# Optimization experiments

Measured on AMD Instinct MI355X. Metric: run time of the kernel, lower is better.

Reference implementation:

```python
import jax, jax.numpy as jnp
import numpy as np

N_GRAPHS = 128   # number of graphs in the batch
G = 128          # nodes per graph (equal-sized ragged blocks for the reference)
D = 512          # node embedding dim (feature_dim)
EPS = 1e-7


def setup_inputs() -> dict:
    key = jax.random.key(0)
    embeddings = jax.random.normal(key, (N_GRAPHS * G, D), dtype=jnp.float32)
    # Precompute block-diagonal strict-upper-triangular mask as gather indices.
    # Equivalent to torch.block_diag(*[triu(ones(g,g), diagonal=1) for g in sizes]).bool()
    iu_r, iu_c = np.triu_indices(G, k=1)                 # per-block triu(.,1) indices
    offsets = (np.arange(N_GRAPHS) * G)[:, None]         # block offsets into [N, N]
    row_idx = jnp.asarray((offsets + iu_r[None, :]).ravel(), dtype=jnp.int32)
    col_idx = jnp.asarray((offsets + iu_c[None, :]).ravel(), dtype=jnp.int32)
    return {"embeddings": embeddings, "row_idx": row_idx, "col_idx": col_idx}


def reference(embeddings, row_idx, col_idx):
    # Full NxN dot-product similarity (N = total nodes across all graphs).
    sims = embeddings @ embeddings.T                     # [N, N]
    m = sims.min()
    M = sims.max()
    sims = (sims - m) / (M - m + EPS)                    # global min-max normalization
    # Gather block-diagonal strict-upper-triangular entries -> flat vector.
    return sims[row_idx, col_idx]                        # [sum_g g*(g-1)/2]
```

## Files before the change

### kernel.cpp

```cpp
#include <hip/hip_runtime.h>
#include <hip/hip_bf16.h>
#include <stdint.h>


typedef __attribute__((ext_vector_type(8))) __bf16 bf16x8;
typedef __attribute__((ext_vector_type(16))) float floatx16;
typedef __attribute__((ext_vector_type(4))) int intx4;
typedef __attribute__((ext_vector_type(16))) int intx16;

#define AS1 __attribute__((address_space(1)))
#define AS3 __attribute__((address_space(3)))

static constexpr int DIM      = 512;
static constexpr int SLOTX    = 40;
static constexpr int NSLOT    = SLOTX * 64;
static constexpr float QS     = 19.5f;
static constexpr int MARGIN_I = 3042;


static __device__ __forceinline__ unsigned short f2bf_rne(float f) {
  unsigned int u = __float_as_uint(f);
  u += 0x7fffu + ((u >> 16) & 1u);
  return (unsigned short)(u >> 16);
}
static __device__ __forceinline__ int fkey(float f) {
  int s = __float_as_int(f);
  return s >= 0 ? s : (s ^ 0x7fffffff);
}
static __device__ __forceinline__ float funkey(int k) {
  return __int_as_float(k >= 0 ? k : (k ^ 0x7fffffff));
}
static __device__ __forceinline__ int swzd(int row, int c16) {
  return c16 ^ (row & 15);
}
static __device__ __forceinline__ int swz8(int row, int c8) {
  return c8 ^ (row & 7);
}
static __device__ __forceinline__ int qswap(int v) {
  return (v & 0x7A) | ((v & 1) << 2) | ((v >> 2) & 1);
}
static __device__ __forceinline__ int sfun(int row) {
  return (row & 3) ^ ((row >> 3) & 3);
}

__global__ void k_convert(const float* __restrict__ in,
                          unsigned short* __restrict__ bf,
                          char* __restrict__ q,
                          int* __restrict__ ctrl, int n4) {
  int i = blockIdx.x * blockDim.x + threadIdx.x;
  if (i == 0) {
    ctrl[0] = 0x7fffffff; ctrl[1] = (int)0x80000000;
    ctrl[2] = 0x7fffffff;
  }
  if (i >= n4) return;
  float4 v = ((const float4*)in)[i];
  ushort4 o;
  o.x = f2bf_rne(v.x); o.y = f2bf_rne(v.y);
  o.z = f2bf_rne(v.z); o.w = f2bf_rne(v.w);
  ((ushort4*)bf)[i] = o;
  int qx = __float2int_rn(v.x * QS), qy = __float2int_rn(v.y * QS);
  int qz = __float2int_rn(v.z * QS), qw = __float2int_rn(v.w * QS);
  char4 c;
  c.x = (char)min(127, max(-127, qx));
  c.y = (char)min(127, max(-127, qy));
  c.z = (char)min(127, max(-127, qz));
  c.w = (char)min(127, max(-127, qw));
  ((char4*)q)[i] = c;
}

__global__ __launch_bounds__(512, 2) void k_gemm(
    const char* __restrict__ Eq,
    const unsigned short* __restrict__ E,
    int* __restrict__ ipart,
    float* __restrict__ diagblocks,
    int* __restrict__ ctrl) {
  const int x = blockIdx.x;
  const int y = blockIdx.y;
  if (x > 34) return;
  const int pi = y * SLOTX + x;

  const int tid = threadIdx.x;
  __shared__ __align__(16) char smem[2][32768];
  __shared__ float2 redbuf[8];
  __shared__ int iredbuf[8];

  const int w = tid >> 6, lane = tid & 63;
  const int l31 = lane & 31;
  const int kg  = lane >> 5;

  if (x < 33) {
    const int tt = (y + x) & 63;
    const int rA0 = 256 * y,  rA1 = 256 * y + 128;
    const int rB0 = 256 * tt, rB1 = 256 * tt + 128;

    const int wr = w >> 1, wc = w & 1;

    intx16 acc[2][4];
#pragma unroll
    for (int i = 0; i < 2; i++)
#pragma unroll
      for (int j = 0; j < 4; j++)
#pragma unroll
        for (int r = 0; r < 16; r++) acc[i][j][r] = 0;

#define STAGE4(bb, kt) do {                                                   \
    int q_   = tid >> 2;                                                      \
    int row_ = qswap(q_);                                                     \
    int off_ = (kt) * 64 + (((tid & 3) ^ sfun(row_)) * 16);                   \
    char* d_ = smem[bb] + tid * 16;                                           \
    __builtin_amdgcn_global_load_lds(                                         \
        (const AS1 unsigned int*)(Eq + (size_t)(rA0 + row_) * DIM + off_),    \
        (AS3 unsigned int*)d_, 16, 0, 0);                                     \
    __builtin_amdgcn_global_load_lds(                                         \
        (const AS1 unsigned int*)(Eq + (size_t)(rA1 + row_) * DIM + off_),    \
        (AS3 unsigned int*)(d_ + 8192), 16, 0, 0);                            \
    __builtin_amdgcn_global_load_lds(                                         \
        (const AS1 unsigned int*)(Eq + (size_t)(rB0 + row_) * DIM + off_),    \
        (AS3 unsigned int*)(d_ + 16384), 16, 0, 0);                           \
    __builtin_amdgcn_global_load_lds(                                         \
        (const AS1 unsigned int*)(Eq + (size_t)(rB1 + row_) * DIM + off_),    \
        (AS3 unsigned int*)(d_ + 24576), 16, 0, 0);                           \
  } while (0)

    const int ra0 = wr * 64 + l31, ra1 = wr * 64 + 32 + l31;
    const int pa0 = (ra0 >> 7) * 8192 + qswap(ra0 & 127) * 64, sa0 = sfun(ra0 & 127);
    const int pa1 = (ra1 >> 7) * 8192 + qswap(ra1 & 127) * 64, sa1 = sfun(ra1 & 127);
    const int rb0 = 0 * 32 + l31, rb1 = 1 * 32 + l31;
    const int rb2 = 2 * 32 + l31, rb3 = 3 * 32 + l31;
    const int pbB = 16384 + wc * 8192;
    const int pb0 = pbB + qswap(rb0) * 64, sb0 = sfun(rb0);
    const int pb1 = pbB + qswap(rb1) * 64, sb1 = sfun(rb1);
    const int pb2 = pbB + qswap(rb2) * 64, sb2 = sfun(rb2);
    const int pb3 = pbB + qswap(rb3) * 64, sb3 = sfun(rb3);

    STAGE4(0, 0);
    __syncthreads();

#pragma unroll
    for (int kt = 0; kt < 8; kt++) {
      if (kt + 1 < 8) STAGE4((kt + 1) & 1, kt + 1);
      const char* cb = smem[kt & 1];
#pragma unroll
      for (int ks = 0; ks < 2; ks++) {
        const int c = ks * 2 + kg;
        intx4 af0 = *(const intx4*)(cb + pa0 + ((c ^ sa0) << 4));
        intx4 af1 = *(const intx4*)(cb + pa1 + ((c ^ sa1) << 4));
        intx4 b0  = *(const intx4*)(cb + pb0 + ((c ^ sb0) << 4));
        intx4 b1  = *(const intx4*)(cb + pb1 + ((c ^ sb1) << 4));
        intx4 b2  = *(const intx4*)(cb + pb2 + ((c ^ sb2) << 4));
        intx4 b3  = *(const intx4*)(cb + pb3 + ((c ^ sb3) << 4));
        acc[0][0] = __builtin_amdgcn_mfma_i32_32x32x32_i8(af0, b0, acc[0][0], 0, 0, 0);
        acc[0][1] = __builtin_amdgcn_mfma_i32_32x32x32_i8(af0, b1, acc[0][1], 0, 0, 0);
        acc[0][2] = __builtin_amdgcn_mfma_i32_32x32x32_i8(af0, b2, acc[0][2], 0, 0, 0);
        acc[0][3] = __builtin_amdgcn_mfma_i32_32x32x32_i8(af0, b3, acc[0][3], 0, 0, 0);
        acc[1][0] = __builtin_amdgcn_mfma_i32_32x32x32_i8(af1, b0, acc[1][0], 0, 0, 0);
        acc[1][1] = __builtin_amdgcn_mfma_i32_32x32x32_i8(af1, b1, acc[1][1], 0, 0, 0);
        acc[1][2] = __builtin_amdgcn_mfma_i32_32x32x32_i8(af1, b2, acc[1][2], 0, 0, 0);
        acc[1][3] = __builtin_amdgcn_mfma_i32_32x32x32_i8(af1, b3, acc[1][3], 0, 0, 0);
      }
      __syncthreads();
    }
#undef STAGE4

    int vmin = 0x7fffffff;
#pragma unroll
    for (int ti = 0; ti < 2; ti++)
#pragma unroll
      for (int tj = 0; tj < 4; tj++)
#pragma unroll
        for (int r = 0; r < 16; r++) vmin = min(vmin, acc[ti][tj][r]);
#pragma unroll
    for (int m_ = 32; m_ >= 1; m_ >>= 1)
      vmin = min(vmin, __shfl_xor(vmin, m_));
    if (lane == 0) iredbuf[w] = vmin;
    __syncthreads();
    if (tid == 0) {
      int mn = iredbuf[0];
      for (int i = 1; i < 8; i++) mn = min(mn, iredbuf[i]);
      ipart[pi] = mn;
      atomicMin(&ctrl[2], mn);
    }
  } else {
    if (tid == 0) ipart[pi] = 0x7fffffff;
    const int tr = 2 * y + (x - 33);
    unsigned short* lA = (unsigned short*)&smem[0][0];
    const int wr = w >> 2, wcq = w & 3;
    floatx16 acc[2];
#pragma unroll
    for (int t = 0; t < 2; t++)
#pragma unroll
      for (int r = 0; r < 16; r++) acc[t][r] = 0.f;

    const int rowBase = tr * 128;

    for (int kb = 0; kb < 4; kb++) {
      const int kBase = kb * 128;
#pragma unroll
      for (int j = 0; j < 4; j++) {
        int p   = j * 512 + tid;
        int row = p >> 4, c16 = p & 15;
        int sc = swzd(row, c16);
        const unsigned short* gA =
            E + (size_t)(rowBase + row) * DIM + kBase + sc * 8;
        __builtin_amdgcn_global_load_lds((const AS1 unsigned int*)gA,
                                         (AS3 unsigned int*)(lA + p * 8), 16, 0, 0);
      }
      __syncthreads();

#pragma unroll
      for (int ks = 0; ks < 8; ks++) {
        bf16x8 af[2], bfv;
        const int c16 = ks * 2 + kg;
#pragma unroll
        for (int t = 0; t < 2; t++) {
          int ra = wr * 64 + t * 32 + l31;
          af[t]  = *(const bf16x8*)(lA + ra * 128 + swzd(ra, c16) * 8);
        }
        {
          int rb = wcq * 32 + l31;
          bfv = *(const bf16x8*)(lA + rb * 128 + swzd(rb, c16) * 8);
        }
#pragma unroll
        for (int t = 0; t < 2; t++)
          acc[t] = __builtin_amdgcn_mfma_f32_32x32x16_bf16(
              af[t], bfv, acc[t], 0, 0, 0);
      }
      __syncthreads();
    }

    float vmin = 3.4e38f, vmax = -3.4e38f;
#pragma unroll
    for (int t = 0; t < 2; t++)
#pragma unroll
      for (int r = 0; r < 16; r++) {
        float v = acc[t][r];
        vmin = fminf(vmin, v);
        vmax = fmaxf(vmax, v);
      }
#pragma unroll
    for (int m_ = 32; m_ >= 1; m_ >>= 1) {
      vmin = fminf(vmin, __shfl_xor(vmin, m_));
      vmax = fmaxf(vmax, __shfl_xor(vmax, m_));
    }
    if (lane == 0) redbuf[w] = make_float2(vmin, vmax);
    __syncthreads();
    if (tid == 0) {
      float mn = redbuf[0].x, mx = redbuf[0].y;
      for (int i = 1; i < 8; i++) {
        mn = fminf(mn, redbuf[i].x);
        mx = fmaxf(mx, redbuf[i].y);
      }
      atomicMin(&ctrl[0], fkey(mn));
      atomicMax(&ctrl[1], fkey(mx));
    }

    float* Bout = diagblocks + (size_t)tr * (128 * 128);
    const int cbase = wcq * 32 + l31;
#pragma unroll
    for (int t = 0; t < 2; t++) {
#pragma unroll
      for (int r = 0; r < 16; r++) {
        int row = wr * 64 + t * 32 + (r & 3) + 8 * (r >> 2) + 4 * kg;
        Bout[row * 128 + cbase] = acc[t][r];
      }
    }
  }
}

__global__ __launch_bounds__(256) void k_refine(
    const unsigned short* __restrict__ E,
    const int* __restrict__ ipart, int* __restrict__ ctrl) {
  const int pi = blockIdx.x;
  if (ipart[pi] > ctrl[2] + MARGIN_I) return;
  const int y = pi / SLOTX, x = pi % SLOTX;
  if (x >= 33) return;
  const int tt = (y + x) & 63;

  const int tid = threadIdx.x;
  __shared__ __align__(16) unsigned short lA[128 * 64];
  __shared__ __align__(16) unsigned short lB[128 * 64];
  __shared__ float redbuf[4];

  const int w = tid >> 6, lane = tid & 63;
  const int wr = w >> 1, wc = w & 1;
  const int l31 = lane & 31;
  const int kg  = lane >> 5;

  for (int ab = 0; ab < 4; ab++) {
    const int rowBaseA = (2 * y + (ab >> 1)) * 128;
    const int rowBaseB = (2 * tt + (ab & 1)) * 128;

    floatx16 acc[2][2];
#pragma unroll
    for (int i = 0; i < 2; i++)
#pragma unroll
      for (int j = 0; j < 2; j++)
#pragma unroll
        for (int r = 0; r < 16; r++) acc[i][j][r] = 0.f;

    for (int kb = 0; kb < 8; kb++) {
      const int kBase = kb * 64;
#pragma unroll
      for (int j = 0; j < 4; j++) {
        int cb  = (w * 4 + j) * 64;
        int p   = cb + lane;
        int row = p >> 3, c8 = p & 7;
        int sc8 = swz8(row, c8);
        const unsigned short* gA = E + (size_t)(rowBaseA + row) * DIM + kBase + sc8 * 8;
        const unsigned short* gB = E + (size_t)(rowBaseB + row) * DIM + kBase + sc8 * 8;
        __builtin_amdgcn_global_load_lds((const AS1 unsigned int*)gA,
                                         (AS3 unsigned int*)(lA + cb * 8), 16, 0, 0);
        __builtin_amdgcn_global_load_lds((const AS1 unsigned int*)gB,
                                         (AS3 unsigned int*)(lB + cb * 8), 16, 0, 0);
      }
      __syncthreads();

#pragma unroll
      for (int ks = 0; ks < 4; ks++) {
        bf16x8 af[2], bfv[2];
        const int c8 = ks * 2 + kg;
#pragma unroll
        for (int t = 0; t < 2; t++) {
          int ra = wr * 64 + t * 32 + l31;
          int rb = wc * 64 + t * 32 + l31;
          af[t]  = *(const bf16x8*)(lA + (ra * 8 + swz8(ra, c8)) * 8);
          bfv[t] = *(const bf16x8*)(lB + (rb * 8 + swz8(rb, c8)) * 8);
        }
#pragma unroll
        for (int ti = 0; ti < 2; ti++)
#pragma unroll
          for (int tj = 0; tj < 2; tj++)
            acc[ti][tj] = __builtin_amdgcn_mfma_f32_32x32x16_bf16(
                af[ti], bfv[tj], acc[ti][tj], 0, 0, 0);
      }
      __syncthreads();
    }

    float vmin = 3.4e38f;
#pragma unroll
    for (int ti = 0; ti < 2; ti++)
#pragma unroll
      for (int tj = 0; tj < 2; tj++)
#pragma unroll
        for (int r = 0; r < 16; r++) vmin = fminf(vmin, acc[ti][tj][r]);
#pragma unroll
    for (int m_ = 32; m_ >= 1; m_ >>= 1)
      vmin = fminf(vmin, __shfl_xor(vmin, m_));
    if (lane == 0) redbuf[w] = vmin;
    __syncthreads();
    if (tid == 0) {
      float mn = redbuf[0];
      for (int i = 1; i < 4; i++) mn = fminf(mn, redbuf[i]);
      atomicMin(&ctrl[0], fkey(mn));
    }
    __syncthreads();
  }
}

__global__ __launch_bounds__(256) void k_gather(
    const int* __restrict__ rix, const int* __restrict__ cix,
    const float* __restrict__ blocks, const int* __restrict__ ctrl,
    float* __restrict__ out, int n) {
  int i = blockIdx.x * blockDim.x + threadIdx.x;
  if (i >= n) return;
  float m   = funkey(ctrl[0]);
  float M   = funkey(ctrl[1]);
  float inv = 1.0f / (M - m + 1e-7f);
  int r = rix[i], c = cix[i];
  int g = r >> 7;
  float v = blocks[((size_t)g << 14) + ((r & 127) << 7) + (c & 127)];
  out[i] = (v - m) * inv;
}

extern "C" void kernel_launch(void* const* d_in, const int* in_sizes, int n_in,
                              void* d_out, int out_size, void* d_ws, size_t ws_size,
                              hipStream_t stream) {
  const float* emb = (const float*)d_in[0];
  const int* rix   = (const int*)d_in[1];
  const int* cix   = (const int*)d_in[2];

  char* ws = (char*)d_ws;
  int* ctrl           = (int*)ws;
  unsigned short* Ebf = (unsigned short*)(ws + 256);
  char* Eq            = (char*)(ws + 256 + (16u << 20));
  float* diagblocks   = (float*)(ws + 256 + (24u << 20));
  int* ipart          = (int*)(ws + 256 + (32u << 20));
  int n4 = in_sizes[0] / 4;

  k_convert<<<(n4 + 255) / 256, 256, 0, stream>>>(emb, Ebf, Eq, ctrl, n4);

  k_gemm<<<dim3(SLOTX, 64), 512, 0, stream>>>(Eq, Ebf, ipart, diagblocks, ctrl);

  k_refine<<<NSLOT, 256, 0, stream>>>(Ebf, ipart, ctrl);

  k_gather<<<(out_size + 255) / 256, 256, 0, stream>>>(rix, cix, diagblocks,
                                                       ctrl, (float*)d_out,
                                                       out_size);
}
```

Baseline: 200.1 us.

## Triple-buffer int8 GEMM tiles with split staging and explicit waitcnt barriers

Moves the int8 GEMM mainloop from double to triple LDS buffering. Tiles are now prefetched two k-steps ahead, and each stage's global-to-LDS loads are split across the two inner k-substeps. __syncthreads is replaced with manual s_barrier, vmcnt/lgkmcnt waits, sched_barrier and setprio around the MFMA bursts, to hide load latency and interleave loads with compute. The cost is 96KB of LDS per block, which may cut occupancy below the two blocks per CU requested by launch_bounds, plus fragile hand-tuned wait counts.

After: 206.0 us. +2.9%, slower.

```diff
diff --git a/kernel.cpp b/kernel.cpp
--- a/kernel.cpp
+++ b/kernel.cpp
@@ -80,7 +80,7 @@
   const int pi = y * SLOTX + x;
 
   const int tid = threadIdx.x;
-  __shared__ __align__(16) char smem[2][32768];
+  __shared__ __align__(16) char smem[3][32768];
   __shared__ float2 redbuf[8];
   __shared__ int iredbuf[8];
 
@@ -103,23 +103,26 @@
 #pragma unroll
         for (int r = 0; r < 16; r++) acc[i][j][r] = 0;
 
-#define STAGE4(bb, kt) do {                                                   \
+#define STAGE2(bb, kt, h) do {                                                \
     int q_   = tid >> 2;                                                      \
     int row_ = qswap(q_);                                                     \
     int off_ = (kt) * 64 + (((tid & 3) ^ sfun(row_)) * 16);                   \
     char* d_ = smem[bb] + tid * 16;                                           \
-    __builtin_amdgcn_global_load_lds(                                         \
-        (const AS1 unsigned int*)(Eq + (size_t)(rA0 + row_) * DIM + off_),    \
-        (AS3 unsigned int*)d_, 16, 0, 0);                                     \
-    __builtin_amdgcn_global_load_lds(                                         \
-        (const AS1 unsigned int*)(Eq + (size_t)(rA1 + row_) * DIM + off_),    \
-        (AS3 unsigned int*)(d_ + 8192), 16, 0, 0);                            \
-    __builtin_amdgcn_global_load_lds(                                         \
-        (const AS1 unsigned int*)(Eq + (size_t)(rB0 + row_) * DIM + off_),    \
-        (AS3 unsigned int*)(d_ + 16384), 16, 0, 0);                           \
-    __builtin_amdgcn_global_load_lds(                                         \
-        (const AS1 unsigned int*)(Eq + (size_t)(rB1 + row_) * DIM + off_),    \
-        (AS3 unsigned int*)(d_ + 24576), 16, 0, 0);                           \
+    if ((h) == 0) {                                                           \
+      __builtin_amdgcn_global_load_lds(                                       \
+          (const AS1 unsigned int*)(Eq + (size_t)(rA0 + row_) * DIM + off_),  \
+          (AS3 unsigned int*)d_, 16, 0, 0);                                   \
+      __builtin_amdgcn_global_load_lds(                                       \
+          (const AS1 unsigned int*)(Eq + (size_t)(rA1 + row_) * DIM + off_),  \
+          (AS3 unsigned int*)(d_ + 8192), 16, 0, 0);                          \
+    } else {                                                                  \
+      __builtin_amdgcn_global_load_lds(                                       \
+          (const AS1 unsigned int*)(Eq + (size_t)(rB0 + row_) * DIM + off_),  \
+          (AS3 unsigned int*)(d_ + 16384), 16, 0, 0);                         \
+      __builtin_amdgcn_global_load_lds(                                       \
+          (const AS1 unsigned int*)(Eq + (size_t)(rB1 + row_) * DIM + off_),  \
+          (AS3 unsigned int*)(d_ + 24576), 16, 0, 0);                         \
+    }                                                                         \
   } while (0)
 
     const int ra0 = wr * 64 + l31, ra1 = wr * 64 + 32 + l31;
@@ -133,13 +136,15 @@
     const int pb2 = pbB + qswap(rb2) * 64, sb2 = sfun(rb2);
     const int pb3 = pbB + qswap(rb3) * 64, sb3 = sfun(rb3);
 
-    STAGE4(0, 0);
-    __syncthreads();
+    STAGE2(0, 0, 0); STAGE2(0, 0, 1);
+    STAGE2(1, 1, 0); STAGE2(1, 1, 1);
+    asm volatile("s_waitcnt vmcnt(4)" ::: "memory");
+    __builtin_amdgcn_s_barrier();
+    __builtin_amdgcn_sched_barrier(0);
 
 #pragma unroll
     for (int kt = 0; kt < 8; kt++) {
-      if (kt + 1 < 8) STAGE4((kt + 1) & 1, kt + 1);
-      const char* cb = smem[kt & 1];
+      const char* cb = smem[kt % 3];
 #pragma unroll
       for (int ks = 0; ks < 2; ks++) {
         const int c = ks * 2 + kg;
@@ -149,6 +154,11 @@
         intx4 b1  = *(const intx4*)(cb + pb1 + ((c ^ sb1) << 4));
         intx4 b2  = *(const intx4*)(cb + pb2 + ((c ^ sb2) << 4));
         intx4 b3  = *(const intx4*)(cb + pb3 + ((c ^ sb3) << 4));
+        if (kt + 2 < 8) STAGE2((kt + 2) % 3, kt + 2, ks);
+        __builtin_amdgcn_s_barrier();
+        asm volatile("s_waitcnt lgkmcnt(0)" ::: "memory");
+        __builtin_amdgcn_sched_barrier(0);
+        __builtin_amdgcn_s_setprio(1);
         acc[0][0] = __builtin_amdgcn_mfma_i32_32x32x32_i8(af0, b0, acc[0][0], 0, 0, 0);
         acc[0][1] = __builtin_amdgcn_mfma_i32_32x32x32_i8(af0, b1, acc[0][1], 0, 0, 0);
         acc[0][2] = __builtin_amdgcn_mfma_i32_32x32x32_i8(af0, b2, acc[0][2], 0, 0, 0);
@@ -157,10 +167,17 @@
         acc[1][1] = __builtin_amdgcn_mfma_i32_32x32x32_i8(af1, b1, acc[1][1], 0, 0, 0);
         acc[1][2] = __builtin_amdgcn_mfma_i32_32x32x32_i8(af1, b2, acc[1][2], 0, 0, 0);
         acc[1][3] = __builtin_amdgcn_mfma_i32_32x32x32_i8(af1, b3, acc[1][3], 0, 0, 0);
-      }
-      __syncthreads();
-    }
-#undef STAGE4
+        __builtin_amdgcn_s_setprio(0);
+        __builtin_amdgcn_sched_barrier(0);
+        if (ks == 1) {
+          if (kt < 6)       { asm volatile("s_waitcnt vmcnt(4)" ::: "memory"); }
+          else if (kt == 6) { asm volatile("s_waitcnt vmcnt(0)" ::: "memory"); }
+        }
+        __builtin_amdgcn_s_barrier();
+        __builtin_amdgcn_sched_barrier(0);
+      }
+    }
+#undef STAGE2
 
     int vmin = 0x7fffffff;
 #pragma unroll
```
